# Kernel optimization log

Measured on AMD Instinct MI355X. Metric: run time of the kernel, lower is better.

Reference implementation:

```python
import jax, jax.numpy as jnp
import numpy as np

H = 16
D_MODEL = 1024
D_K = D_MODEL // H
NEG = -1e9


def setup_inputs() -> dict:
    key = jax.random.key(0)
    ks = jax.random.split(key, 12)
    B, S, D = 2, 2048, D_MODEL
    scale = 1.0 / np.sqrt(D)
    inp = {
        "query": jax.random.normal(ks[0], (B, S, D), jnp.float32),
        "key": jax.random.normal(ks[1], (B, S, D), jnp.float32),
        "value": jax.random.normal(ks[2], (B, S, D), jnp.float32),
        "mask": jax.random.randint(ks[3], (B, S, S), 0, 2, jnp.int32),
        # four Linear(d_model, d_model) layers: q, k, v, out projections
        "Wq": jax.random.normal(ks[4], (D, D), jnp.float32) * scale,
        "bq": jnp.zeros((D,), jnp.float32),
        "Wk": jax.random.normal(ks[5], (D, D), jnp.float32) * scale,
        "bk": jnp.zeros((D,), jnp.float32),
        "Wv": jax.random.normal(ks[6], (D, D), jnp.float32) * scale,
        "bv": jnp.zeros((D,), jnp.float32),
        "Wo": jax.random.normal(ks[7], (D, D), jnp.float32) * scale,
        "bo": jnp.zeros((D,), jnp.float32),
    }
    return inp


def reference(query, key, value, mask, Wq, bq, Wk, bk, Wv, bv, Wo, bo):
    B, S, D = query.shape
    # QKV projections, then split into heads: [B, H, S, D_K]
    def proj(x, W, b):
        return (x @ W + b).reshape(B, S, H, D_K).transpose(0, 2, 1, 3)

    q = proj(query, Wq, bq)
    k = proj(key, Wk, bk)
    v = proj(value, Wv, bv)

    # scaled dot-product attention; scale by sqrt(d_k) (query.size(-1) after split)
    scores = jnp.einsum("bhqd,bhkd->bhqk", q, k) / np.sqrt(D_K)
    scores = jnp.where(mask[:, None, :, :] == 0, NEG, scores)
    p = jax.nn.softmax(scores, axis=-1)  # dropout is identity in eval mode
    x = jnp.einsum("bhqk,bhkd->bhqd", p, v)

    # merge heads and apply output projection
    x = x.transpose(0, 2, 1, 3).reshape(B, S, H * D_K)
    return x @ Wo + bo
```

## Files before the change

kernel.cpp:

```cpp
#include <hip/hip_runtime.h>

typedef _Float16 f16;
typedef __attribute__((ext_vector_type(2))) _Float16 f16x2;
typedef __attribute__((ext_vector_type(4))) _Float16 f16x4;
typedef __attribute__((ext_vector_type(8))) _Float16 f16x8;
typedef __attribute__((ext_vector_type(4))) float f32x4;

#define MFMA16(A_, B_, C_) __builtin_amdgcn_mfma_f32_16x16x32_f16(A_, B_, C_, 0, 0, 0)
#define EXP2(x) __builtin_amdgcn_exp2f(x)

#define NHEAD 16
#define SEQ 2048
#define DM 1024
#define DK 64
#define NBATCH 2
#define M_TOT (NBATCH * SEQ)
#define CSC 0.18033688011112042f

#define GLDS(gp, lp)                                                                     \
    __builtin_amdgcn_global_load_lds((const __attribute__((address_space(1))) void*)(gp), \
                                     (__attribute__((address_space(3))) void*)(lp), 16, 0, 0)

__global__ __launch_bounds__(256) void prep_k(
    const int* __restrict__ mask, unsigned long long* __restrict__ mp,
    const float* __restrict__ xq, const float* __restrict__ xk, const float* __restrict__ xv,
    f16* __restrict__ oq, f16* __restrict__ ok, f16* __restrict__ ov,
    const float* __restrict__ Wq, const float* __restrict__ Wk,
    const float* __restrict__ Wv, const float* __restrict__ Wo, f16* __restrict__ Wt) {
    __shared__ float T[64][65];
    const int z = blockIdx.z, bx = blockIdx.x, tid = threadIdx.x;
    if (z < 3) {
        const float* src = z == 0 ? xq : (z == 1 ? xk : xv);
        f16* dst = z == 0 ? oq : (z == 1 ? ok : ov);
        size_t i = ((size_t)bx * 256 + tid) * 8;
        float4 a = *(const float4*)&src[i];
        float4 b = *(const float4*)&src[i + 4];
        f16x8 h;
        h[0] = (f16)a.x; h[1] = (f16)a.y; h[2] = (f16)a.z; h[3] = (f16)a.w;
        h[4] = (f16)b.x; h[5] = (f16)b.y; h[6] = (f16)b.z; h[7] = (f16)b.w;
        *(f16x8*)&dst[i] = h;
    } else if (z == 3) {
        if (bx >= 1024) return;
        const int zz = bx >> 8, t = bx & 255;
        const float* W = zz == 0 ? Wq : (zz == 1 ? Wk : (zz == 2 ? Wv : Wo));
        const float wsc = zz == 0 ? CSC : 1.0f;
        f16* out = Wt + (size_t)zz * DM * DM;
        const int k0 = (t >> 4) * 64, n0 = (t & 15) * 64;
        const int r = tid >> 2, q = tid & 3;
        const float4* s = (const float4*)&W[(size_t)(k0 + r) * DM + n0 + q * 16];
        float4 v0 = s[0], v1 = s[1], v2 = s[2], v3 = s[3];
        T[r][q * 16 + 0] = v0.x; T[r][q * 16 + 1] = v0.y; T[r][q * 16 + 2] = v0.z; T[r][q * 16 + 3] = v0.w;
        T[r][q * 16 + 4] = v1.x; T[r][q * 16 + 5] = v1.y; T[r][q * 16 + 6] = v1.z; T[r][q * 16 + 7] = v1.w;
        T[r][q * 16 + 8] = v2.x; T[r][q * 16 + 9] = v2.y; T[r][q * 16 + 10] = v2.z; T[r][q * 16 + 11] = v2.w;
        T[r][q * 16 + 12] = v3.x; T[r][q * 16 + 13] = v3.y; T[r][q * 16 + 14] = v3.z; T[r][q * 16 + 15] = v3.w;
        __syncthreads();
        f16x8 h0, h1;
#pragma unroll
        for (int j = 0; j < 8; ++j) {
            h0[j] = (f16)(T[q * 16 + j][r] * wsc);
            h1[j] = (f16)(T[q * 16 + 8 + j][r] * wsc);
        }
        *(f16x8*)&out[(size_t)(n0 + r) * DM + k0 + q * 16] = h0;
        *(f16x8*)&out[(size_t)(n0 + r) * DM + k0 + q * 16 + 8] = h1;
    } else {
        if (bx >= 512) return;
        int lane = tid & 63;
        int gw = (bx * 256 + tid) >> 6;
        const int nw = (512 * 256) >> 6;
        const int nwords = NBATCH * SEQ * (SEQ / 64);
        for (int w = gw; w < nwords; w += nw) {
            int v = mask[(size_t)w * 64 + lane];
            unsigned long long bits = __ballot(v != 0);
            if (lane == 0) mp[w] = bits;
        }
    }
}

__device__ __forceinline__ void gemm_core(const f16* __restrict__ A, const f16* __restrict__ Bt,
                                          int m0, int n0, f16* Al, f16* Bl, f32x4 acc[4][4], int tid) {
    const int lane = tid & 63;
    const int wv = tid >> 6;
    const int wr = wv >> 1, wc = wv & 1;
    const int g = lane >> 4, c = lane & 15;

    for (int k0 = 0; k0 < DM; k0 += 64) {
#pragma unroll
        for (int j = 0; j < 4; ++j) {
            int chunk = j * 256 + tid;
            int row = chunk >> 3, cc = chunk & 7;
            int ccs = cc ^ (row & 7);
            GLDS(&A[(size_t)(m0 + row) * DM + k0 + ccs * 8], &Al[chunk * 8]);
        }
#pragma unroll
        for (int j = 0; j < 4; ++j) {
            int chunk = j * 256 + tid;
            int row = chunk >> 3, cc = chunk & 7;
            int ccs = cc ^ (row & 7);
            GLDS(&Bt[(size_t)(n0 + row) * DM + k0 + ccs * 8], &Bl[chunk * 8]);
        }
        __syncthreads();
#pragma unroll
        for (int ks = 0; ks < 2; ++ks) {
            f16x8 af[4], bf[4];
#pragma unroll
            for (int mi = 0; mi < 4; ++mi) {
                int row = wr * 64 + mi * 16 + c;
                af[mi] = *(const f16x8*)&Al[row * 64 + ((ks * 4 + g) ^ (row & 7)) * 8];
            }
#pragma unroll
            for (int ni = 0; ni < 4; ++ni) {
                int row = wc * 64 + ni * 16 + c;
                bf[ni] = *(const f16x8*)&Bl[row * 64 + ((ks * 4 + g) ^ (row & 7)) * 8];
            }
#pragma unroll
            for (int mi = 0; mi < 4; ++mi)
#pragma unroll
                for (int ni = 0; ni < 4; ++ni)
                    acc[mi][ni] = MFMA16(af[mi], bf[ni], acc[mi][ni]);
        }
        __syncthreads();
    }
}

__global__ __launch_bounds__(256) void gemm_qkv2_k(
    const f16* __restrict__ Xq, const f16* __restrict__ Xk, const f16* __restrict__ Xv,
    const f16* __restrict__ Wt, const float* __restrict__ bq, const float* __restrict__ bk,
    const float* __restrict__ bv, f16* __restrict__ Qh, f16* __restrict__ Kh, f16* __restrict__ VhT) {
    __shared__ f16 Al[128 * 64];
    __shared__ f16 Bl[128 * 64];
    const int which = blockIdx.z;
    const f16* A = which == 0 ? Xq : (which == 1 ? Xk : Xv);
    const f16* Bt = Wt + (size_t)which * DM * DM;
    const float* bias = which == 0 ? bq : (which == 1 ? bk : bv);

    const int tid = threadIdx.x, lane = tid & 63, wv = tid >> 6;
    const int wr = wv >> 1, wc = wv & 1, g = lane >> 4, c = lane & 15;
    const int m0 = blockIdx.y * 128, n0 = blockIdx.x * 128;

    f32x4 acc[4][4] = {};
    gemm_core(A, Bt, m0, n0, Al, Bl, acc, tid);

    const float bsc = which == 0 ? CSC : 1.0f;
    if (which == 2) {
#pragma unroll
        for (int ni = 0; ni < 4; ++ni) {
            int n = n0 + wc * 64 + ni * 16 + c;
            float bias_n = bias[n];
            int hh = n >> 6, d = n & 63;
#pragma unroll
            for (int mi = 0; mi < 4; ++mi) {
                int mbase = m0 + wr * 64 + mi * 16 + g * 4;
                int bb = mbase >> 11, s = mbase & (SEQ - 1);
                f16x4 o;
#pragma unroll
                for (int r = 0; r < 4; ++r) o[r] = (f16)(acc[mi][ni][r] + bias_n);
                *(f16x4*)&VhT[(((size_t)(bb * NHEAD + hh)) * DK + d) * SEQ + s] = o;
            }
        }
    } else {
        f16* OUT = which == 0 ? Qh : Kh;
#pragma unroll
        for (int ni = 0; ni < 4; ++ni) {
            int n = n0 + wc * 64 + ni * 16 + c;
            float bias_n = bias[n] * bsc;
            int hh = n >> 6, d = n & 63;
#pragma unroll
            for (int mi = 0; mi < 4; ++mi) {
                int mbase = m0 + wr * 64 + mi * 16 + g * 4;
#pragma unroll
                for (int r = 0; r < 4; ++r) {
                    int m = mbase + r;
                    int bb = m >> 11, s = m & (SEQ - 1);
                    OUT[(((size_t)(bb * NHEAD + hh)) * SEQ + s) * DK + d] = (f16)(acc[mi][ni][r] + bias_n);
                }
            }
        }
    }
}

__global__ __launch_bounds__(256) void gemm_out2_k(
    const f16* __restrict__ Xo, const f16* __restrict__ Wto, const float* __restrict__ bo,
    float* __restrict__ OUT) {
    __shared__ f16 Al[128 * 64];
    __shared__ f16 Bl[128 * 64];
    const int tid = threadIdx.x, lane = tid & 63, wv = tid >> 6;
    const int wr = wv >> 1, wc = wv & 1, g = lane >> 4, c = lane & 15;
    const int m0 = blockIdx.y * 128, n0 = blockIdx.x * 128;

    f32x4 acc[4][4] = {};
    gemm_core(Xo, Wto, m0, n0, Al, Bl, acc, tid);

#pragma unroll
    for (int ni = 0; ni < 4; ++ni) {
        int n = n0 + wc * 64 + ni * 16 + c;
        float bias_n = bo[n];
#pragma unroll
        for (int mi = 0; mi < 4; ++mi) {
            int mbase = m0 + wr * 64 + mi * 16 + g * 4;
#pragma unroll
            for (int r = 0; r < 4; ++r) {
                int m = mbase + r;
                OUT[(size_t)m * DM + n] = acc[mi][ni][r] + bias_n;
            }
        }
    }
}

#define QBLK 128
#define NHALF 2
#define KTH (SEQ / 64 / NHALF)
#define PSTR 76

__global__ __launch_bounds__(512) void attn_k(
    const f16* __restrict__ Qh, const f16* __restrict__ Kh, const f16* __restrict__ VhT,
    const unsigned long long* __restrict__ mp, f16* __restrict__ O0, f16* __restrict__ O1,
    float2* __restrict__ ml) {
    __shared__ f16 Kl[2][4096];
    __shared__ f16 Vl[2][4096];
    __shared__ f16 Plds[8][16 * PSTR];

    const int tid = threadIdx.x, lane = tid & 63, wv = tid >> 6;
    const int g = lane >> 4, c = lane & 15;
    const int qt = blockIdx.x, hh = blockIdx.y;
    const int b = blockIdx.z >> 1, half = blockIdx.z & 1;
    const size_t headoff = ((size_t)(b * NHEAD + hh)) * SEQ * DK;
    const f16* Qb = Qh + headoff;
    const f16* Kb = Kh + headoff + (size_t)half * (SEQ / NHALF) * DK;
    const f16* VbT = VhT + headoff + (size_t)half * (SEQ / NHALF);

    const int srow = tid >> 3, scc = (tid & 7) ^ (srow & 7);

#define STAGE_ATTN(jj, pp)                                                      \
    do {                                                                        \
        GLDS(&Kb[(size_t)((jj)*64 + srow) * DK + scc * 8], &Kl[pp][tid * 8]);   \
        GLDS(&VbT[(size_t)srow * SEQ + (jj)*64 + scc * 8], &Vl[pp][tid * 8]);   \
    } while (0)

    const int qrow = qt * QBLK + wv * 16 + c;
    f16x8 bq0 = *(const f16x8*)&Qb[(size_t)qrow * DK + g * 8];
    f16x8 bq1 = *(const f16x8*)&Qb[(size_t)qrow * DK + 32 + g * 8];

    f32x4 acc[4] = {};
    float l_run = 0.f;

    const unsigned long long* mrow = mp + ((size_t)b * SEQ + qrow) * (SEQ / 64) + half * KTH;
    unsigned long long wq_cur = mrow[0];

    STAGE_ATTN(0, 0);
    int p = 0;
    for (int j = 0; j < KTH; ++j) {
        __syncthreads();
        if (j + 1 < KTH) STAGE_ATTN(j + 1, p ^ 1);
        unsigned long long wq_nxt = (j + 1 < KTH) ? mrow[j + 1] : 0ull;

        f32x4 sc[4];
        __builtin_amdgcn_s_setprio(1);
#pragma unroll
        for (int nk = 0; nk < 4; ++nk) {
            int row = nk * 16 + c;
            f16x8 k0 = *(const f16x8*)&Kl[p][row * 64 + ((g ^ (row & 7)) * 8)];
            f16x8 k1 = *(const f16x8*)&Kl[p][row * 64 + (((4 + g) ^ (row & 7)) * 8)];
            f32x4 z = {};
            z = MFMA16(k0, bq0, z);
            z = MFMA16(k1, bq1, z);
            sc[nk] = z;
        }
        __builtin_amdgcn_s_setprio(0);

        unsigned long long wq = wq_cur >> (g * 4);
        float ps = 0.f;
#pragma unroll
        for (int nk = 0; nk < 4; ++nk) {
            unsigned int nib = (unsigned int)(wq >> (nk * 16)) & 0xFu;
#pragma unroll
            for (int r = 0; r < 4; ++r) {
                float pp = EXP2(sc[nk][r]);
                pp = (nib & (1u << r)) ? pp : 0.f;
                sc[nk][r] = pp;
                ps += pp;
            }
        }
        l_run += ps;

#pragma unroll
        for (int nk = 0; nk < 4; ++nk)
#pragma unroll
            for (int r2 = 0; r2 < 2; ++r2) {
                f16x2 pw = {(f16)sc[nk][r2 * 2], (f16)sc[nk][r2 * 2 + 1]};
                *(f16x2*)&Plds[wv][c * PSTR + nk * 16 + g * 4 + r2 * 2] = pw;
            }
        f16x8 pb0 = *(const f16x8*)&Plds[wv][c * PSTR + g * 8];
        f16x8 pb1 = *(const f16x8*)&Plds[wv][c * PSTR + 32 + g * 8];

        __builtin_amdgcn_s_setprio(1);
#pragma unroll
        for (int nd = 0; nd < 4; ++nd) {
            int row = nd * 16 + c;
            f16x8 v0 = *(const f16x8*)&Vl[p][row * 64 + ((g ^ (row & 7)) * 8)];
            f16x8 v1 = *(const f16x8*)&Vl[p][row * 64 + (((4 + g) ^ (row & 7)) * 8)];
            acc[nd] = MFMA16(v0, pb0, acc[nd]);
            acc[nd] = MFMA16(v1, pb1, acc[nd]);
        }
        __builtin_amdgcn_s_setprio(0);

        wq_cur = wq_nxt;
        p ^= 1;
    }

    l_run += __shfl_xor(l_run, 16);
    l_run += __shfl_xor(l_run, 32);

    f16* Opart = half ? O1 : O0;
    {
        float inv = l_run > 0.f ? 1.0f / l_run : 0.f;
        size_t hrow = headoff / DK + qrow;
#pragma unroll
        for (int nd = 0; nd < 4; ++nd) {
            f16x4 o;
#pragma unroll
            for (int r = 0; r < 4; ++r) o[r] = (f16)(acc[nd][r] * inv);
            *(f16x4*)&Opart[hrow * DK + nd * 16 + g * 4] = o;
        }
        if (g == 0) ml[(size_t)half * (M_TOT * NHEAD) + hrow] = make_float2(0.f, l_run);
    }
#undef STAGE_ATTN
}

__global__ __launch_bounds__(256) void combine_k(const f16* __restrict__ O0, const f16* __restrict__ O1,
                                                 const float2* __restrict__ ml, f16* __restrict__ Xo) {
    const int row = blockIdx.x * 32 + (threadIdx.x >> 3);
    const int d0 = (threadIdx.x & 7) * 8;
    const int b = row >> 15, hh = (row >> 11) & 15, q = row & (SEQ - 1);
    float2 a = ml[row];
    float2 bb = ml[(M_TOT * NHEAD) + row];
    float m = fmaxf(a.x, bb.x);
    float w0 = a.y * EXP2(a.x - m);
    float w1 = bb.y * EXP2(bb.x - m);
    float inv = 1.0f / (w0 + w1);
    float a0 = w0 * inv, a1 = w1 * inv;
    f16x8 o0 = *(const f16x8*)&O0[(size_t)row * DK + d0];
    f16x8 o1 = *(const f16x8*)&O1[(size_t)row * DK + d0];
    f16x8 o;
#pragma unroll
    for (int i = 0; i < 8; ++i) o[i] = (f16)(a0 * (float)o0[i] + a1 * (float)o1[i]);
    *(f16x8*)&Xo[((size_t)(b * SEQ + q)) * DM + hh * DK + d0] = o;
}

extern "C" void kernel_launch(void* const* d_in, const int* in_sizes, int n_in,
                              void* d_out, int out_size, void* d_ws, size_t ws_size,
                              hipStream_t stream) {
    const float* query = (const float*)d_in[0];
    const float* key_ = (const float*)d_in[1];
    const float* value = (const float*)d_in[2];
    const int* mask = (const int*)d_in[3];
    const float* Wq = (const float*)d_in[4];
    const float* bq = (const float*)d_in[5];
    const float* Wk = (const float*)d_in[6];
    const float* bk = (const float*)d_in[7];
    const float* Wv = (const float*)d_in[8];
    const float* bv = (const float*)d_in[9];
    const float* Wo = (const float*)d_in[10];
    const float* bo = (const float*)d_in[11];
    float* out = (float*)d_out;

    char* ws = (char*)d_ws;
    const size_t headsz = (size_t)NBATCH * NHEAD * SEQ * DK * sizeof(f16);
    unsigned long long* mp = (unsigned long long*)(ws);
    f16* Qh = (f16*)(ws + (1 << 20));
    f16* Kh = (f16*)(ws + (1 << 20) + headsz);
    f16* VhT = (f16*)(ws + (1 << 20) + 2 * headsz);
    f16* Xhq = (f16*)(ws + (1 << 20) + 3 * headsz);
    f16* Xhk = (f16*)(ws + (1 << 20) + 4 * headsz);
    f16* Xhv = (f16*)(ws + (1 << 20) + 5 * headsz);
    f16* Wt = (f16*)(ws + (1 << 20) + 6 * headsz);
    float2* ml = (float2*)(ws + (1 << 20) + 7 * headsz);
    f16* Xo = Xhq;

    hipLaunchKernelGGL(prep_k, dim3(M_TOT * DM / (8 * 256), 1, 5), dim3(256), 0, stream,
                       mask, mp, query, key_, value, Xhq, Xhk, Xhv, Wq, Wk, Wv, Wo, Wt);
    hipLaunchKernelGGL(gemm_qkv2_k, dim3(DM / 128, M_TOT / 128, 3), dim3(256), 0, stream,
                       Xhq, Xhk, Xhv, Wt, bq, bk, bv, Qh, Kh, VhT);
    hipLaunchKernelGGL(attn_k, dim3(SEQ / QBLK, NHEAD, NBATCH * NHALF), dim3(512), 0, stream,
                       Qh, Kh, VhT, mp, Xhk, Xhv, ml);
    hipLaunchKernelGGL(combine_k, dim3(M_TOT * NHEAD / 32), dim3(256), 0, stream, Xhk, Xhv, ml, Xo);
    hipLaunchKernelGGL(gemm_out2_k, dim3(DM / 128, M_TOT / 128), dim3(256), 0, stream,
                       Xo, Wt + (size_t)3 * DM * DM, bo, out);
}
```

Measured before the change: 170.6 us.

## Drop split-KV attention and combine kernel, add XCD block swizzle to GEMMs

Attention now walks the full key sequence in one block per query tile and writes the normalized output straight into the merged-head buffer. This removes the separate combine kernel and its partial-output and statistics round trip through memory. The cost is half as many attention blocks (512 instead of 1024), each with a loop twice as long, which may lower parallelism and latency hiding. Separately, both GEMM kernels remap block indices so that blocks landing on the same XCD work on neighbouring tiles, aiming for better L2 reuse.

```diff
diff --git a/kernel.cpp b/kernel.cpp
--- a/kernel.cpp
+++ b/kernel.cpp
@@ -122,6 +122,13 @@
     }
 }
 
+__device__ __forceinline__ void xcd_swizzle(int& bx, int& by, int gdx) {
+    int lin = by * gdx + bx;
+    int nl = (lin & 7) * 32 + (lin >> 3);
+    bx = nl % gdx;
+    by = nl / gdx;
+}
+
 __global__ __launch_bounds__(256) void gemm_qkv2_k(
     const f16* __restrict__ Xq, const f16* __restrict__ Xk, const f16* __restrict__ Xv,
     const f16* __restrict__ Wt, const float* __restrict__ bq, const float* __restrict__ bk,
@@ -135,7 +142,9 @@
 
     const int tid = threadIdx.x, lane = tid & 63, wv = tid >> 6;
     const int wr = wv >> 1, wc = wv & 1, g = lane >> 4, c = lane & 15;
-    const int m0 = blockIdx.y * 128, n0 = blockIdx.x * 128;
+    int bx = blockIdx.x, by = blockIdx.y;
+    xcd_swizzle(bx, by, gridDim.x);
+    const int m0 = by * 128, n0 = bx * 128;
 
     f32x4 acc[4][4] = {};
     gemm_core(A, Bt, m0, n0, Al, Bl, acc, tid);
@@ -185,7 +194,9 @@
     __shared__ f16 Bl[128 * 64];
     const int tid = threadIdx.x, lane = tid & 63, wv = tid >> 6;
     const int wr = wv >> 1, wc = wv & 1, g = lane >> 4, c = lane & 15;
-    const int m0 = blockIdx.y * 128, n0 = blockIdx.x * 128;
+    int bx = blockIdx.x, by = blockIdx.y;
+    xcd_swizzle(bx, by, gridDim.x);
+    const int m0 = by * 128, n0 = bx * 128;
 
     f32x4 acc[4][4] = {};
     gemm_core(Xo, Wto, m0, n0, Al, Bl, acc, tid);
@@ -207,26 +218,23 @@
 }
 
 #define QBLK 128
-#define NHALF 2
-#define KTH (SEQ / 64 / NHALF)
+#define KT_ALL (SEQ / 64)
 #define PSTR 76
 
 __global__ __launch_bounds__(512) void attn_k(
     const f16* __restrict__ Qh, const f16* __restrict__ Kh, const f16* __restrict__ VhT,
-    const unsigned long long* __restrict__ mp, f16* __restrict__ O0, f16* __restrict__ O1,
-    float2* __restrict__ ml) {
+    const unsigned long long* __restrict__ mp, f16* __restrict__ Xo) {
     __shared__ f16 Kl[2][4096];
     __shared__ f16 Vl[2][4096];
     __shared__ f16 Plds[8][16 * PSTR];
 
     const int tid = threadIdx.x, lane = tid & 63, wv = tid >> 6;
     const int g = lane >> 4, c = lane & 15;
-    const int qt = blockIdx.x, hh = blockIdx.y;
-    const int b = blockIdx.z >> 1, half = blockIdx.z & 1;
+    const int qt = blockIdx.x, hh = blockIdx.y, b = blockIdx.z;
     const size_t headoff = ((size_t)(b * NHEAD + hh)) * SEQ * DK;
     const f16* Qb = Qh + headoff;
-    const f16* Kb = Kh + headoff + (size_t)half * (SEQ / NHALF) * DK;
-    const f16* VbT = VhT + headoff + (size_t)half * (SEQ / NHALF);
+    const f16* Kb = Kh + headoff;
+    const f16* VbT = VhT + headoff;
 
     const int srow = tid >> 3, scc = (tid & 7) ^ (srow & 7);
 
@@ -243,15 +251,15 @@
     f32x4 acc[4] = {};
     float l_run = 0.f;
 
-    const unsigned long long* mrow = mp + ((size_t)b * SEQ + qrow) * (SEQ / 64) + half * KTH;
+    const unsigned long long* mrow = mp + ((size_t)b * SEQ + qrow) * (SEQ / 64);
     unsigned long long wq_cur = mrow[0];
 
     STAGE_ATTN(0, 0);
     int p = 0;
-    for (int j = 0; j < KTH; ++j) {
+    for (int j = 0; j < KT_ALL; ++j) {
         __syncthreads();
-        if (j + 1 < KTH) STAGE_ATTN(j + 1, p ^ 1);
-        unsigned long long wq_nxt = (j + 1 < KTH) ? mrow[j + 1] : 0ull;
+        if (j + 1 < KT_ALL) STAGE_ATTN(j + 1, p ^ 1);
+        unsigned long long wq_nxt = (j + 1 < KT_ALL) ? mrow[j + 1] : 0ull;
 
         f32x4 sc[4];
         __builtin_amdgcn_s_setprio(1);
@@ -310,40 +318,17 @@
     l_run += __shfl_xor(l_run, 16);
     l_run += __shfl_xor(l_run, 32);
 
-    f16* Opart = half ? O1 : O0;
     {
         float inv = l_run > 0.f ? 1.0f / l_run : 0.f;
-        size_t hrow = headoff / DK + qrow;
 #pragma unroll
         for (int nd = 0; nd < 4; ++nd) {
             f16x4 o;
 #pragma unroll
             for (int r = 0; r < 4; ++r) o[r] = (f16)(acc[nd][r] * inv);
-            *(f16x4*)&Opart[hrow * DK + nd * 16 + g * 4] = o;
-        }
-        if (g == 0) ml[(size_t)half * (M_TOT * NHEAD) + hrow] = make_float2(0.f, l_run);
+            *(f16x4*)&Xo[((size_t)(b * SEQ) + qrow) * DM + hh * DK + nd * 16 + g * 4] = o;
+        }
     }
 #undef STAGE_ATTN
-}
-
-__global__ __launch_bounds__(256) void combine_k(const f16* __restrict__ O0, const f16* __restrict__ O1,
-                                                 const float2* __restrict__ ml, f16* __restrict__ Xo) {
-    const int row = blockIdx.x * 32 + (threadIdx.x >> 3);
-    const int d0 = (threadIdx.x & 7) * 8;
-    const int b = row >> 15, hh = (row >> 11) & 15, q = row & (SEQ - 1);
-    float2 a = ml[row];
-    float2 bb = ml[(M_TOT * NHEAD) + row];
-    float m = fmaxf(a.x, bb.x);
-    float w0 = a.y * EXP2(a.x - m);
-    float w1 = bb.y * EXP2(bb.x - m);
-    float inv = 1.0f / (w0 + w1);
-    float a0 = w0 * inv, a1 = w1 * inv;
-    f16x8 o0 = *(const f16x8*)&O0[(size_t)row * DK + d0];
-    f16x8 o1 = *(const f16x8*)&O1[(size_t)row * DK + d0];
-    f16x8 o;
-#pragma unroll
-    for (int i = 0; i < 8; ++i) o[i] = (f16)(a0 * (float)o0[i] + a1 * (float)o1[i]);
-    *(f16x8*)&Xo[((size_t)(b * SEQ + q)) * DM + hh * DK + d0] = o;
 }
 
 extern "C" void kernel_launch(void* const* d_in, const int* in_sizes, int n_in,
@@ -373,16 +358,14 @@
     f16* Xhk = (f16*)(ws + (1 << 20) + 4 * headsz);
     f16* Xhv = (f16*)(ws + (1 << 20) + 5 * headsz);
     f16* Wt = (f16*)(ws + (1 << 20) + 6 * headsz);
-    float2* ml = (float2*)(ws + (1 << 20) + 7 * headsz);
     f16* Xo = Xhq;
 
     hipLaunchKernelGGL(prep_k, dim3(M_TOT * DM / (8 * 256), 1, 5), dim3(256), 0, stream,
                        mask, mp, query, key_, value, Xhq, Xhk, Xhv, Wq, Wk, Wv, Wo, Wt);
     hipLaunchKernelGGL(gemm_qkv2_k, dim3(DM / 128, M_TOT / 128, 3), dim3(256), 0, stream,
                        Xhq, Xhk, Xhv, Wt, bq, bk, bv, Qh, Kh, VhT);
-    hipLaunchKernelGGL(attn_k, dim3(SEQ / QBLK, NHEAD, NBATCH * NHALF), dim3(512), 0, stream,
-                       Qh, Kh, VhT, mp, Xhk, Xhv, ml);
-    hipLaunchKernelGGL(combine_k, dim3(M_TOT * NHEAD / 32), dim3(256), 0, stream, Xhk, Xhv, ml, Xo);
+    hipLaunchKernelGGL(attn_k, dim3(SEQ / QBLK, NHEAD, NBATCH), dim3(512), 0, stream,
+                       Qh, Kh, VhT, mp, Xo);
     hipLaunchKernelGGL(gemm_out2_k, dim3(DM / 128, M_TOT / 128), dim3(256), 0, stream,
                        Xo, Wt + (size_t)3 * DM * DM, bo, out);
 }
```

After: 159.4 us. 6.5% less time.

## Permute K rows to keep P in registers and swizzle blocks across XCDs

Applied to the files above, without the earlier changes.

The attention kernel now loads K rows in a permuted order so the score MFMA output layout matches the B-operand layout of the PV MFMA. P can then be packed directly from registers instead of round-tripping through a per-wave LDS buffer, and the mask nibble extraction is adjusted to the permuted key order. The GEMM kernels remap block indices so consecutive tiles land on the same XCD, and the attention grid is flattened so blocks sharing a head/batch group map to the same XCD for L2 reuse. This saves LDS traffic and a sync-free store/load per iteration, at the cost of more intricate index math that must stay consistent with the mask packing.

```diff
diff --git a/kernel.cpp b/kernel.cpp
--- a/kernel.cpp
+++ b/kernel.cpp
@@ -122,6 +122,13 @@
     }
 }
 
+__device__ __forceinline__ void xcd_swizzle(int& bx, int& by, int gdx) {
+    int lin = by * gdx + bx;
+    int nl = (lin & 7) * 32 + (lin >> 3);
+    bx = nl % gdx;
+    by = nl / gdx;
+}
+
 __global__ __launch_bounds__(256) void gemm_qkv2_k(
     const f16* __restrict__ Xq, const f16* __restrict__ Xk, const f16* __restrict__ Xv,
     const f16* __restrict__ Wt, const float* __restrict__ bq, const float* __restrict__ bk,
@@ -135,7 +142,9 @@
 
     const int tid = threadIdx.x, lane = tid & 63, wv = tid >> 6;
     const int wr = wv >> 1, wc = wv & 1, g = lane >> 4, c = lane & 15;
-    const int m0 = blockIdx.y * 128, n0 = blockIdx.x * 128;
+    int bx = blockIdx.x, by = blockIdx.y;
+    xcd_swizzle(bx, by, gridDim.x);
+    const int m0 = by * 128, n0 = bx * 128;
 
     f32x4 acc[4][4] = {};
     gemm_core(A, Bt, m0, n0, Al, Bl, acc, tid);
@@ -185,7 +194,9 @@
     __shared__ f16 Bl[128 * 64];
     const int tid = threadIdx.x, lane = tid & 63, wv = tid >> 6;
     const int wr = wv >> 1, wc = wv & 1, g = lane >> 4, c = lane & 15;
-    const int m0 = blockIdx.y * 128, n0 = blockIdx.x * 128;
+    int bx = blockIdx.x, by = blockIdx.y;
+    xcd_swizzle(bx, by, gridDim.x);
+    const int m0 = by * 128, n0 = bx * 128;
 
     f32x4 acc[4][4] = {};
     gemm_core(Xo, Wto, m0, n0, Al, Bl, acc, tid);
@@ -209,7 +220,6 @@
 #define QBLK 128
 #define NHALF 2
 #define KTH (SEQ / 64 / NHALF)
-#define PSTR 76
 
 __global__ __launch_bounds__(512) void attn_k(
     const f16* __restrict__ Qh, const f16* __restrict__ Kh, const f16* __restrict__ VhT,
@@ -217,22 +227,25 @@
     float2* __restrict__ ml) {
     __shared__ f16 Kl[2][4096];
     __shared__ f16 Vl[2][4096];
-    __shared__ f16 Plds[8][16 * PSTR];
 
     const int tid = threadIdx.x, lane = tid & 63, wv = tid >> 6;
     const int g = lane >> 4, c = lane & 15;
-    const int qt = blockIdx.x, hh = blockIdx.y;
-    const int b = blockIdx.z >> 1, half = blockIdx.z & 1;
+    const int lin = blockIdx.x;
+    const int key = lin & 31;
+    const int half = (lin >> 5) & 1;
+    const int qt = lin >> 6;
+    const int hh = key & (NHEAD - 1), b = key >> 4;
     const size_t headoff = ((size_t)(b * NHEAD + hh)) * SEQ * DK;
     const f16* Qb = Qh + headoff;
     const f16* Kb = Kh + headoff + (size_t)half * (SEQ / NHALF) * DK;
     const f16* VbT = VhT + headoff + (size_t)half * (SEQ / NHALF);
 
     const int srow = tid >> 3, scc = (tid & 7) ^ (srow & 7);
+    const int kap = ((srow >> 4) & 1) * 32 + ((srow >> 2) & 3) * 8 + ((srow >> 5) & 1) * 4 + (srow & 3);
 
 #define STAGE_ATTN(jj, pp)                                                      \
     do {                                                                        \
-        GLDS(&Kb[(size_t)((jj)*64 + srow) * DK + scc * 8], &Kl[pp][tid * 8]);   \
+        GLDS(&Kb[(size_t)((jj)*64 + kap) * DK + scc * 8], &Kl[pp][tid * 8]);    \
         GLDS(&VbT[(size_t)srow * SEQ + (jj)*64 + scc * 8], &Vl[pp][tid * 8]);   \
     } while (0)
 
@@ -267,11 +280,11 @@
         }
         __builtin_amdgcn_s_setprio(0);
 
-        unsigned long long wq = wq_cur >> (g * 4);
+        unsigned long long wq_g = wq_cur >> (g * 8);
         float ps = 0.f;
 #pragma unroll
         for (int nk = 0; nk < 4; ++nk) {
-            unsigned int nib = (unsigned int)(wq >> (nk * 16)) & 0xFu;
+            unsigned int nib = (unsigned int)(wq_g >> ((nk & 1) * 32 + (nk >> 1) * 4)) & 0xFu;
 #pragma unroll
             for (int r = 0; r < 4; ++r) {
                 float pp = EXP2(sc[nk][r]);
@@ -282,15 +295,14 @@
         }
         l_run += ps;
 
-#pragma unroll
-        for (int nk = 0; nk < 4; ++nk)
-#pragma unroll
-            for (int r2 = 0; r2 < 2; ++r2) {
-                f16x2 pw = {(f16)sc[nk][r2 * 2], (f16)sc[nk][r2 * 2 + 1]};
-                *(f16x2*)&Plds[wv][c * PSTR + nk * 16 + g * 4 + r2 * 2] = pw;
-            }
-        f16x8 pb0 = *(const f16x8*)&Plds[wv][c * PSTR + g * 8];
-        f16x8 pb1 = *(const f16x8*)&Plds[wv][c * PSTR + 32 + g * 8];
+        f16x8 pb0, pb1;
+#pragma unroll
+        for (int j2 = 0; j2 < 2; ++j2)
+#pragma unroll
+            for (int r = 0; r < 4; ++r) {
+                pb0[j2 * 4 + r] = (f16)sc[j2 * 2][r];
+                pb1[j2 * 4 + r] = (f16)sc[j2 * 2 + 1][r];
+            }
 
         __builtin_amdgcn_s_setprio(1);
 #pragma unroll
@@ -380,7 +392,7 @@
                        mask, mp, query, key_, value, Xhq, Xhk, Xhv, Wq, Wk, Wv, Wo, Wt);
     hipLaunchKernelGGL(gemm_qkv2_k, dim3(DM / 128, M_TOT / 128, 3), dim3(256), 0, stream,
                        Xhq, Xhk, Xhv, Wt, bq, bk, bv, Qh, Kh, VhT);
-    hipLaunchKernelGGL(attn_k, dim3(SEQ / QBLK, NHEAD, NBATCH * NHALF), dim3(512), 0, stream,
+    hipLaunchKernelGGL(attn_k, dim3(SEQ / QBLK * NHEAD * NBATCH * NHALF), dim3(512), 0, stream,
                        Qh, Kh, VhT, mp, Xhk, Xhv, ml);
     hipLaunchKernelGGL(combine_k, dim3(M_TOT * NHEAD / 32), dim3(256), 0, stream, Xhk, Xhv, ml, Xo);
     hipLaunchKernelGGL(gemm_out2_k, dim3(DM / 128, M_TOT / 128), dim3(256), 0, stream,
```

New measurement: 159.1 us. 1.07x faster.
